# Kernel tuning notes

Hardware: AMD Instinct MI355X
Metric: run time of the kernel (lower is better)

The kernel has to match this reference:

```python
import jax, jax.numpy as jnp
import numpy as np

MAX_LAB = 64  # cap on connected-component ids per sample (original cc3d is unbounded)
BIG = jnp.int32(2 ** 30)


def _cc_label(mask):
    """26-connectivity connected components of a 3D bool mask via label propagation.
    Each component ends with label == max initial voxel id in it (nonzero), bg = 0."""
    n = mask.size
    init = jnp.where(mask, jnp.arange(1, n + 1, dtype=jnp.int32).reshape(mask.shape), jnp.int32(0))

    def cond(st):
        return jnp.any(st[0] != st[1])

    def body(st):
        lab = st[0]
        # max over 3x3x3 neighborhood == 26-connectivity propagation step
        neigh = jax.lax.reduce_window(lab, jnp.int32(0), jax.lax.max, (3, 3, 3), (1, 1, 1), 'SAME')
        return (jnp.where(mask, neigh, jnp.int32(0)), lab)

    lab, _ = jax.lax.while_loop(cond, body, (init, jnp.full_like(init, -1)))
    return lab


def _compact(lab):
    """Relabel a per-sample label map to consecutive ids 0,1..k (0 = background),
    matching cc3d's 1..k numbering."""
    u = jnp.unique(lab, size=MAX_LAB + 1, fill_value=BIG)  # sorted: [0, l1, .., lk, BIG..]
    return jnp.searchsorted(u, lab).astype(jnp.int32)


def _instance_dice(x, y):
    xb = jnp.squeeze(x, 1) > 0.5  # [B,D,H,W] pred foreground
    yb = jnp.squeeze(y, 1) > 0.5  # [B,D,H,W] gt foreground
    label = jax.vmap(lambda m: _compact(_cc_label(m)))
    gt_lab = label(yb)  # per-sample ids 0..k_i (ids shared across batch, as in original)
    pr_lab = label(xb)
    M = MAX_LAB + 1
    # joint histogram over (gt component id, pred component id), global across batch
    idx = gt_lab.reshape(-1) * M + pr_lab.reshape(-1)
    overlap = jax.ops.segment_sum(jnp.ones(idx.shape, jnp.float32), idx, num_segments=M * M).reshape(M, M)
    gt_size = overlap.sum(1)  # [M] voxels per gt id
    pr_size = overlap.sum(0)  # [M] voxels per pred id
    ov = overlap[1:, 1:]                       # [G,P] fg-fg overlaps
    inter_mask = ov > 0                        # pred comp p intersects gt comp g
    inter = ov.sum(1)                          # [G] |gt_g  ∩  union(intersecting preds)|
    union_sz = (inter_mask * pr_size[1:]).sum(1)  # [G] |union of intersecting pred comps|
    has_inter = inter > 0
    dice = jnp.where(has_inter, 2.0 * inter / jnp.maximum(union_sz + gt_size[1:], 1.0), 0.0)
    lesion_dice = dice.sum()
    num_gt = jnp.sum(gt_size[1:] > 0).astype(jnp.float32)
    tp_mask = inter_mask.any(0)                # [P] pred comps matched to some gt
    num_fp = jnp.sum((pr_size[1:] > 0) & ~tp_mask).astype(jnp.float32)
    return lesion_dice / (num_gt + num_fp)


def setup_inputs() -> dict:
    B, D, H, W = 2, 128, 128, 128
    R, N_BLOBS = 5, 12
    rng = np.random.default_rng(0)
    zz, yy, xx = np.meshgrid(np.arange(D), np.arange(H), np.arange(W), indexing='ij')

    def blobs(k):
        m = np.zeros((B, D, H, W), bool)
        for b in range(B):
            c = rng.integers(R + 2, D - R - 2, size=(k, 3))
            for cz, cy, cx in c:
                m[b] |= (zz - cz) ** 2 + (yy - cy) ** 2 + (xx - cx) ** 2 <= R * R
        return m

    y = blobs(N_BLOBS)
    # prediction = slightly shifted gt (partial-overlap TPs) + extra false-positive blobs
    x = np.roll(y, shift=(2, 1, 0), axis=(1, 2, 3)) | blobs(4)
    return {"x": jnp.asarray(x[:, None].astype(np.float32)),
            "y": jnp.asarray(y[:, None].astype(np.float32))}


def reference(x, y):
    return _instance_dice(x, y)
```

## Files before the change

### kernel.cpp

```cpp
#include <hip/hip_runtime.h>


#define NVOX (128 * 128 * 128)
#define NTOT (2 * NVOX)
#define NBLK 4096
#define CAP 12288
#define ML 65
#define NSLAB 8
#define ZSLAB 16
#define EDGE_CAP 8192
#define OVBLK 48

__global__ __launch_bounds__(256) void k_count(
    const float4* __restrict__ x, const float4* __restrict__ y,
    unsigned char* __restrict__ maskArr, int* __restrict__ blkCnt,
    int* __restrict__ overlap, int* __restrict__ cnt) {
    int t = blockIdx.x * 256 + threadIdx.x;
    float4 xv = x[t];
    float4 yv = y[t];
    unsigned m = 0;
    if (xv.x > 0.5f) m |= 1u;
    if (xv.y > 0.5f) m |= 2u;
    if (xv.z > 0.5f) m |= 4u;
    if (xv.w > 0.5f) m |= 8u;
    if (yv.x > 0.5f) m |= 16u;
    if (yv.y > 0.5f) m |= 32u;
    if (yv.z > 0.5f) m |= 64u;
    if (yv.w > 0.5f) m |= 128u;
    maskArr[t] = (unsigned char)m;
    int v = __popc(m & 0xFu) | (__popc(m >> 4) << 16);
    #pragma unroll
    for (int d = 1; d < 64; d <<= 1) v += __shfl_xor(v, d);
    __shared__ int ws[4];
    if ((threadIdx.x & 63) == 0) ws[threadIdx.x >> 6] = v;
    __syncthreads();
    if (threadIdx.x == 0) blkCnt[blockIdx.x] = ws[0] + ws[1] + ws[2] + ws[3];
    if (blockIdx.x == 0) {
        for (int i = threadIdx.x; i < ML * ML; i += 256) overlap[i] = 0;
        if (threadIdx.x < 16) cnt[8 + threadIdx.x] = 0;
    }
}

__global__ __launch_bounds__(256) void k_fill(
    const unsigned char* __restrict__ maskArr, const int* __restrict__ blkCnt,
    int* __restrict__ blkOff, int* __restrict__ cnt,
    unsigned short* __restrict__ posMapX, unsigned short* __restrict__ posMapY,
    int* __restrict__ lists) {
    int blk = blockIdx.x;
    int tid = threadIdx.x;
    int lane = tid & 63, wave = tid >> 6;

    int A = 0, B = 0, C = 0;
    #pragma unroll
    for (int k = 0; k < 4; ++k) {
        int4 c4 = ((const int4*)blkCnt)[tid * 4 + k];
        int i0 = tid * 16 + k * 4;
        const int* cc = &c4.x;
        #pragma unroll
        for (int j = 0; j < 4; ++j) {
            int c = cc[j];
            int i = i0 + j;
            C += c;
            if (i < 2048) B += c;
            if (i < blk)  A += c;
        }
    }
    #pragma unroll
    for (int d = 1; d < 64; d <<= 1) {
        A += __shfl_xor(A, d);
        B += __shfl_xor(B, d);
        C += __shfl_xor(C, d);
    }
    __shared__ int rA[4], rB[4], rC[4];
    if (lane == 0) { rA[wave] = A; rB[wave] = B; rC[wave] = C; }
    __syncthreads();
    A = rA[0] + rA[1] + rA[2] + rA[3];
    B = rB[0] + rB[1] + rB[2] + rB[3];
    C = rC[0] + rC[1] + rC[2] + rC[3];
    int base = A - (blk >= 2048 ? B : 0);
    if (tid == 0) {
        blkOff[blk] = base;
        if (blk == 0) {
            cnt[0] = B & 0xFFFF;
            cnt[2] = B >> 16;
            cnt[1] = (C & 0xFFFF) - (B & 0xFFFF);
            cnt[3] = (C >> 16)    - (B >> 16);
        }
    }

    int t = blk * 256 + tid;
    int b = blk >> 11;
    unsigned m = maskArr[t];
    int px = __popc(m & 0xFu), py = __popc(m >> 4);
    int v = px | (py << 16);
    #pragma unroll
    for (int d = 1; d < 64; d <<= 1) {
        int u = __shfl_up(v, d);
        if (lane >= d) v += u;
    }
    __shared__ int wsum[4];
    if (lane == 63) wsum[wave] = v;
    __syncthreads();
    int woff = 0;
    for (int k = 0; k < wave; ++k) woff += wsum[k];
    int incl = v + woff;
    int baseX = (base & 0xFFFF) + (incl & 0xFFFF) - px;
    int baseY = (base >> 16)    + (incl >> 16)    - py;
    int i = t << 2;
    int j = i & (NVOX - 1);
    ushort4 pxv, pyv;
    unsigned short* ppx = &pxv.x;
    unsigned short* ppy = &pyv.x;
    int cx = 0, cy = 0;
    #pragma unroll
    for (int k = 0; k < 4; ++k) {
        unsigned short vx = 0, vy = 0;
        if (m & (1u << k)) {
            int pos = baseX + cx++;
            if (pos < CAP) { lists[(0 + b) * CAP + pos] = j + k; vx = (unsigned short)(pos + 1); }
        }
        if (m & (1u << (k + 4))) {
            int pos = baseY + cy++;
            if (pos < CAP) { lists[(2 + b) * CAP + pos] = j + k; vy = (unsigned short)(pos + 1); }
        }
        ppx[k] = vx;
        ppy[k] = vy;
    }
    ((ushort4*)posMapX)[t] = pxv;
    ((ushort4*)posMapY)[t] = pyv;
}

__device__ __forceinline__ int find_root(volatile unsigned* parent, int i) {
    unsigned p = parent[i];
    while (p != (unsigned)i) {
        unsigned gp = parent[p];
        if (gp != p) parent[i] = gp;
        i = (int)p;
        p = gp;
    }
    return i;
}

__device__ __forceinline__ void lds_union(unsigned* parentNV, int a, int b) {
    volatile unsigned* parent = (volatile unsigned*)parentNV;
    int ra = find_root(parent, a);
    int rb = find_root(parent, b);
    while (ra != rb) {
        int lo = ra < rb ? ra : rb;
        int hi = ra < rb ? rb : ra;
        unsigned old = atomicCAS(&parentNV[lo], (unsigned)lo, (unsigned)hi);
        if (old == (unsigned)lo) return;
        ra = find_root(parent, (int)old);
        rb = find_root(parent, hi);
    }
}

__device__ __forceinline__ int rank_of(const int* sortedL, int nr, int v) {
    int lo = 0, hi = nr;
    while (lo < hi) { int mid = (lo + hi) >> 1; if (sortedL[mid] < v) lo = mid + 1; else hi = mid; }
    return lo;
}

__global__ __launch_bounds__(1024) void k_cc(
    const unsigned short* __restrict__ posMapX, const unsigned short* __restrict__ posMapY,
    const int* __restrict__ lists, const int* __restrict__ blkOff,
    int* __restrict__ cnt, int* __restrict__ rootPos, int* __restrict__ edges,
    unsigned char* __restrict__ lab8) {
    int fb = blockIdx.y;
    int slab = blockIdx.x;
    int f = fb >> 1, b = fb & 1;
    const unsigned short* posMap = (f ? posMapY : posMapX) + (b << 21);
    const int* fgl = lists + fb * CAP;
    int n = cnt[fb]; if (n > CAP) n = CAP;
    int blkbase = b * 2048 + slab * 256;
    int o0 = blkOff[blkbase];
    int s0 = f ? (o0 >> 16) : (o0 & 0xFFFF);
    int s1;
    if (slab == NSLAB - 1) s1 = n;
    else { int o1 = blkOff[blkbase + 256]; s1 = f ? (o1 >> 16) : (o1 & 0xFFFF); }
    if (s1 > n) s1 = n;
    int ns = s1 - s0;

    __shared__ unsigned parent[CAP];
    __shared__ int slabRoots[1024];
    __shared__ int rootsL[128];
    __shared__ int sortedL[64];
    __shared__ int nsrSh, nrSh, lastFlag;
    int tid = threadIdx.x;
    int lane = tid & 63;

    if (ns > 0) {
        int iters = (ns + 1023) >> 10;

        for (int it = 0; it < iters; ++it) {
            int q = it * 1024 + tid;
            if (q < ns) {
                int p = s0 + q;
                int j = fgl[p];
                unsigned par = (unsigned)q;
                if (p + 1 < s1 && (j & 127) != 127) {
                    if (fgl[p + 1] == j + 1) par = (unsigned)(q + 1);
                }
                parent[q] = par;
            }
        }
        __syncthreads();

        for (int it = 0; it < iters; ++it) {
            int q = it * 1024 + tid;
            bool active = q < ns;
            int j = active ? fgl[s0 + q] : -2;
            int z = j >> 14, y = (j >> 7) & 127, x0 = j & 127;
            bool ztop = active && ((z & (ZSLAB - 1)) == (ZSLAB - 1));
            unsigned short qv[12];
            int idx = 0;
            #pragma unroll
            for (int dx = -1; dx <= 1; ++dx) {
                int yy = y + 1, xx = x0 + dx;
                bool ok = active && yy <= 127 && (unsigned)xx <= 127u;
                int nj = (z << 14) + (yy << 7) + xx;
                qv[idx++] = ok ? posMap[nj] : (unsigned short)0;
            }
            #pragma unroll
            for (int dy = -1; dy <= 1; ++dy)
                #pragma unroll
                for (int dx = -1; dx <= 1; ++dx) {
                    int zz = z + 1, yy = y + dy, xx = x0 + dx;
                    bool ok = active && zz <= 127 && (unsigned)yy <= 127u && (unsigned)xx <= 127u;
                    int nj = (zz << 14) + (yy << 7) + xx;
                    qv[idx++] = ok ? posMap[nj] : (unsigned short)0;
                }
            int jprev = __shfl_up(j, 1);
            bool head = (lane == 0) || !active || ((j & 127) == 0) || (jprev != j - 1);

            int ec = 0;
            int myE[6];
            if (active) {
                {
                    int a = qv[0], bq = qv[1], c = qv[2];
                    if (head) {
                        if (a) lds_union(parent, q, a - 1 - s0);
                        else if (bq) lds_union(parent, q, bq - 1 - s0);
                    }
                    if (c && !bq) lds_union(parent, q, c - 1 - s0);
                }
                if (!ztop) {
                    #pragma unroll
                    for (int r = 1; r < 4; ++r) {
                        int a = qv[r * 3], bq = qv[r * 3 + 1], c = qv[r * 3 + 2];
                        if (head) {
                            if (a) lds_union(parent, q, a - 1 - s0);
                            else if (bq) lds_union(parent, q, bq - 1 - s0);
                        }
                        if (c && !bq) lds_union(parent, q, c - 1 - s0);
                    }
                } else {
                    #pragma unroll
                    for (int r = 1; r < 4; ++r) {
                        int a = qv[r * 3], bq = qv[r * 3 + 1], c = qv[r * 3 + 2];
                        if (head) {
                            if (a) myE[ec++] = (s0 + q) | ((a - 1) << 14);
                            else if (bq) myE[ec++] = (s0 + q) | ((bq - 1) << 14);
                        }
                        if (c && !bq) myE[ec++] = (s0 + q) | ((c - 1) << 14);
                    }
                }
            }
            int pref = ec;
            #pragma unroll
            for (int d = 1; d < 64; d <<= 1) {
                int u = __shfl_up(pref, d);
                if (lane >= d) pref += u;
            }
            int total = __shfl(pref, 63);
            if (total > 0) {
                int ebase = 0;
                if (lane == 63) ebase = atomicAdd(cnt + 8 + fb, total);
                ebase = __shfl(ebase, 63);
                int o = ebase + pref - ec;
                for (int k = 0; k < ec; ++k)
                    if (o + k < EDGE_CAP) edges[fb * EDGE_CAP + o + k] = myE[k];
            }
        }
        __syncthreads();

        for (int it = 0; it < iters; ++it) {
            int q = it * 1024 + tid;
            if (q < ns)
                rootPos[fb * CAP + s0 + q] = s0 + find_root((volatile unsigned*)parent, q);
        }
    }
    __syncthreads();

    if (tid == 0) {
        __threadfence();
        lastFlag = (atomicAdd(&cnt[16 + fb], 1) == NSLAB - 1) ? 1 : 0;
        nsrSh = 0; nrSh = 0;
    }
    __syncthreads();
    if (!lastFlag) return;
    __threadfence();

    int ne = atomicAdd(cnt + 8 + fb, 0);
    if (ne > EDGE_CAP) ne = EDGE_CAP;

    for (int p = tid; p < n; p += 1024) {
        unsigned r = (unsigned)rootPos[fb * CAP + p];
        parent[p] = r;
        if (r == (unsigned)p) {
            int s = atomicAdd(&nsrSh, 1);
            if (s < 1024) slabRoots[s] = p;
        }
    }
    __syncthreads();

    for (int e = tid; e < ne; e += 1024) {
        int pk = edges[fb * EDGE_CAP + e];
        lds_union(parent, pk & 0x3FFF, pk >> 14);
    }
    __syncthreads();

    int nsr = nsrSh; if (nsr > 1024) nsr = 1024;
    for (int i = tid; i < nsr; i += 1024) {
        int r = slabRoots[i];
        if (parent[r] == (unsigned)r) {
            int s = atomicAdd(&nrSh, 1);
            if (s < 128) rootsL[s] = r;
        }
    }
    __syncthreads();
    int nr = nrSh; if (nr > 64) nr = 64;
    if (tid < nr) {
        int v = rootsL[tid];
        int r = 0;
        for (int k = 0; k < nr; ++k) r += (rootsL[k] < v) ? 1 : 0;
        sortedL[r] = v;
    }
    __syncthreads();

    for (int i = tid; i < nsr; i += 1024) {
        int r = slabRoots[i];
        int fr = find_root((volatile unsigned*)parent, r);
        lab8[fb * CAP + r] = (unsigned char)(1 + rank_of(sortedL, nr, fr));
    }
}

__device__ __forceinline__ void hist_add_pred(int* ovl, int key, bool valid) {
    unsigned long long remaining = __ballot(valid ? 1 : 0);
    int lane = threadIdx.x & 63;
    while (remaining) {
        int leader = __ffsll(remaining) - 1;
        int lkey = __shfl(key, leader);
        unsigned long long m = __ballot((valid && lkey == key) ? 1 : 0) & remaining;
        if (lane == leader) atomicAdd(&ovl[lkey], (int)__popcll(m));
        remaining &= ~m;
    }
}

__global__ __launch_bounds__(256) void k_overlap_final(
    const unsigned short* __restrict__ posMapX, const unsigned short* __restrict__ posMapY,
    const int* __restrict__ lists, int* __restrict__ cnt,
    const int* __restrict__ rootPos, const unsigned char* __restrict__ lab8,
    int* __restrict__ overlap, float* __restrict__ out) {
    int fb = blockIdx.y;
    int f = fb >> 1, b = fb & 1;
    int n = cnt[fb]; if (n > CAP) n = CAP;
    int t = blockIdx.x * 256 + threadIdx.x;
    bool valid = t < n;
    int key = 0;
    if (valid) {
        int j = lists[fb * CAP + t];
        int gi = (b << 21) + j;
        if (f == 0) {
            int pc = (int)lab8[fb * CAP + rootPos[fb * CAP + t]];
            int q = (int)posMapY[gi];
            int gc = 0;
            if (q) gc = (int)lab8[(2 + b) * CAP + rootPos[(2 + b) * CAP + (q - 1)]];
            key = gc * ML + pc;
        } else {
            if (posMapX[gi] != 0) valid = false;
            else {
                int gc = (int)lab8[fb * CAP + rootPos[fb * CAP + t]];
                key = gc * ML;
            }
        }
    }
    hist_add_pred(overlap, key, valid);

    __shared__ int lastFlag;
    __syncthreads();
    if (threadIdx.x == 0) {
        __threadfence();
        lastFlag = (atomicAdd(&cnt[12], 1) == 4 * OVBLK - 1) ? 1 : 0;
    }
    __syncthreads();
    if (!lastFlag) return;

    __shared__ int O[ML * ML];
    __shared__ float prs[ML];
    __shared__ unsigned char tp[ML];
    __shared__ float diceSh[ML];
    __shared__ int ngSh[ML];
    __shared__ int nfSh[ML];
    int tid = threadIdx.x;
    for (int i = tid; i < ML * ML; i += 256) O[i] = overlap[i];
    __syncthreads();
    if (tid < ML) {
        int s = 0; int any = 0;
        for (int g = 0; g < ML; ++g) {
            int o = O[g * ML + tid];
            s += o;
            if (g >= 1 && o > 0) any = 1;
        }
        prs[tid] = (float)s;
        tp[tid] = (unsigned char)any;
    }
    __syncthreads();
    if (tid < ML) {
        float dice = 0.f; int ng = 0, nf = 0;
        if (tid >= 1) {
            int gt = 0, inter = 0; float un = 0.f;
            for (int p = 0; p < ML; ++p) {
                int o = O[tid * ML + p];
                gt += o;
                if (p >= 1) { inter += o; if (o > 0) un += prs[p]; }
            }
            if (inter > 0) {
                float den = un + (float)gt;
                if (den < 1.f) den = 1.f;
                dice = 2.f * (float)inter / den;
            }
            ng = (gt > 0) ? 1 : 0;
            nf = (prs[tid] > 0.f && tp[tid] == 0) ? 1 : 0;
        }
        diceSh[tid] = dice; ngSh[tid] = ng; nfSh[tid] = nf;
    }
    __syncthreads();
    if (tid == 0) {
        float ld = 0.f; int ng = 0, nf = 0;
        for (int k = 1; k < ML; ++k) { ld += diceSh[k]; ng += ngSh[k]; nf += nfSh[k]; }
        out[0] = ld / (float)(ng + nf);
    }
}

extern "C" void kernel_launch(void* const* d_in, const int* in_sizes, int n_in,
                              void* d_out, int out_size, void* d_ws, size_t ws_size,
                              hipStream_t stream) {
    const float* x = (const float*)d_in[0];
    const float* y = (const float*)d_in[1];
    float* out = (float*)d_out;

    char* base = (char*)d_ws;
    int* cnt            = (int*)base;
    int* overlap        = cnt + 32;
    int* blkCnt         = overlap + ML * ML;
    int* blkOff         = blkCnt + NBLK;
    int* lists          = blkOff + NBLK;
    int* rootPos        = lists + 4 * CAP;
    int* edges          = rootPos + 4 * CAP;
    unsigned char* lab8 = (unsigned char*)(edges + 4 * EDGE_CAP);
    unsigned char* maskArr = lab8 + 4 * CAP;
    size_t off = (size_t)((maskArr + NTOT / 4) - (unsigned char*)base);
    off = (off + 15) & ~(size_t)15;
    unsigned short* posMapX = (unsigned short*)(base + off);
    unsigned short* posMapY = posMapX + NTOT;

    k_count<<<NBLK, 256, 0, stream>>>((const float4*)x, (const float4*)y,
                                      maskArr, blkCnt, overlap, cnt);
    k_fill<<<NBLK, 256, 0, stream>>>(maskArr, blkCnt, blkOff, cnt,
                                     posMapX, posMapY, lists);
    k_cc<<<dim3(NSLAB, 4), 1024, 0, stream>>>(posMapX, posMapY, lists, blkOff,
                                              cnt, rootPos, edges, lab8);
    k_overlap_final<<<dim3(OVBLK, 4), 256, 0, stream>>>(
        posMapX, posMapY, lists, cnt, rootPos, lab8, overlap, out);
}
```

Baseline: 150.2 us.

## Split CC into finer-slab local kernel and separate merge kernel

```diff
diff --git a/kernel.cpp b/kernel.cpp
--- a/kernel.cpp
+++ b/kernel.cpp
@@ -6,8 +6,9 @@
 #define NBLK 4096
 #define CAP 12288
 #define ML 65
-#define NSLAB 8
-#define ZSLAB 16
+#define NSLAB 16
+#define ZSLAB 8
+#define SLABBLK 128
 #define EDGE_CAP 8192
 #define OVBLK 48
 
@@ -161,149 +162,146 @@
     return lo;
 }
 
-__global__ __launch_bounds__(1024) void k_cc(
+__global__ __launch_bounds__(512) void k_cc_local(
     const unsigned short* __restrict__ posMapX, const unsigned short* __restrict__ posMapY,
     const int* __restrict__ lists, const int* __restrict__ blkOff,
-    int* __restrict__ cnt, int* __restrict__ rootPos, int* __restrict__ edges,
-    unsigned char* __restrict__ lab8) {
+    int* __restrict__ cnt, int* __restrict__ rootPos, int* __restrict__ edges) {
     int fb = blockIdx.y;
     int slab = blockIdx.x;
     int f = fb >> 1, b = fb & 1;
     const unsigned short* posMap = (f ? posMapY : posMapX) + (b << 21);
     const int* fgl = lists + fb * CAP;
     int n = cnt[fb]; if (n > CAP) n = CAP;
-    int blkbase = b * 2048 + slab * 256;
+    int blkbase = b * 2048 + slab * SLABBLK;
     int o0 = blkOff[blkbase];
     int s0 = f ? (o0 >> 16) : (o0 & 0xFFFF);
     int s1;
     if (slab == NSLAB - 1) s1 = n;
-    else { int o1 = blkOff[blkbase + 256]; s1 = f ? (o1 >> 16) : (o1 & 0xFFFF); }
+    else { int o1 = blkOff[blkbase + SLABBLK]; s1 = f ? (o1 >> 16) : (o1 & 0xFFFF); }
     if (s1 > n) s1 = n;
     int ns = s1 - s0;
+    if (ns <= 0) return;
 
     __shared__ unsigned parent[CAP];
-    __shared__ int slabRoots[1024];
-    __shared__ int rootsL[128];
-    __shared__ int sortedL[64];
-    __shared__ int nsrSh, nrSh, lastFlag;
     int tid = threadIdx.x;
     int lane = tid & 63;
-
-    if (ns > 0) {
-        int iters = (ns + 1023) >> 10;
-
-        for (int it = 0; it < iters; ++it) {
-            int q = it * 1024 + tid;
-            if (q < ns) {
-                int p = s0 + q;
-                int j = fgl[p];
-                unsigned par = (unsigned)q;
-                if (p + 1 < s1 && (j & 127) != 127) {
-                    if (fgl[p + 1] == j + 1) par = (unsigned)(q + 1);
-                }
-                parent[q] = par;
-            }
-        }
-        __syncthreads();
-
-        for (int it = 0; it < iters; ++it) {
-            int q = it * 1024 + tid;
-            bool active = q < ns;
-            int j = active ? fgl[s0 + q] : -2;
-            int z = j >> 14, y = (j >> 7) & 127, x0 = j & 127;
-            bool ztop = active && ((z & (ZSLAB - 1)) == (ZSLAB - 1));
-            unsigned short qv[12];
-            int idx = 0;
+    int iters = (ns + 511) >> 9;
+
+    for (int it = 0; it < iters; ++it) {
+        int q = it * 512 + tid;
+        if (q < ns) {
+            int p = s0 + q;
+            int j = fgl[p];
+            unsigned par = (unsigned)q;
+            if (p + 1 < s1 && (j & 127) != 127) {
+                if (fgl[p + 1] == j + 1) par = (unsigned)(q + 1);
+            }
+            parent[q] = par;
+        }
+    }
+    __syncthreads();
+
+    for (int it = 0; it < iters; ++it) {
+        int q = it * 512 + tid;
+        bool active = q < ns;
+        int j = active ? fgl[s0 + q] : -2;
+        int z = j >> 14, y = (j >> 7) & 127, x0 = j & 127;
+        bool ztop = active && ((z & (ZSLAB - 1)) == (ZSLAB - 1));
+        unsigned short qv[12];
+        int idx = 0;
+        #pragma unroll
+        for (int dx = -1; dx <= 1; ++dx) {
+            int yy = y + 1, xx = x0 + dx;
+            bool ok = active && yy <= 127 && (unsigned)xx <= 127u;
+            int nj = (z << 14) + (yy << 7) + xx;
+            qv[idx++] = ok ? posMap[nj] : (unsigned short)0;
+        }
+        #pragma unroll
+        for (int dy = -1; dy <= 1; ++dy)
             #pragma unroll
             for (int dx = -1; dx <= 1; ++dx) {
-                int yy = y + 1, xx = x0 + dx;
-                bool ok = active && yy <= 127 && (unsigned)xx <= 127u;
-                int nj = (z << 14) + (yy << 7) + xx;
+                int zz = z + 1, yy = y + dy, xx = x0 + dx;
+                bool ok = active && zz <= 127 && (unsigned)yy <= 127u && (unsigned)xx <= 127u;
+                int nj = (zz << 14) + (yy << 7) + xx;
                 qv[idx++] = ok ? posMap[nj] : (unsigned short)0;
             }
-            #pragma unroll
-            for (int dy = -1; dy <= 1; ++dy)
+        int jprev = __shfl_up(j, 1);
+        bool head = (lane == 0) || !active || ((j & 127) == 0) || (jprev != j - 1);
+
+        int ec = 0;
+        int myE[6];
+        if (active) {
+            {
+                int a = qv[0], bq = qv[1], c = qv[2];
+                if (head) {
+                    if (a) lds_union(parent, q, a - 1 - s0);
+                    else if (bq) lds_union(parent, q, bq - 1 - s0);
+                }
+                if (c && !bq) lds_union(parent, q, c - 1 - s0);
+            }
+            if (!ztop) {
                 #pragma unroll
-                for (int dx = -1; dx <= 1; ++dx) {
-                    int zz = z + 1, yy = y + dy, xx = x0 + dx;
-                    bool ok = active && zz <= 127 && (unsigned)yy <= 127u && (unsigned)xx <= 127u;
-                    int nj = (zz << 14) + (yy << 7) + xx;
-                    qv[idx++] = ok ? posMap[nj] : (unsigned short)0;
-                }
-            int jprev = __shfl_up(j, 1);
-            bool head = (lane == 0) || !active || ((j & 127) == 0) || (jprev != j - 1);
-
-            int ec = 0;
-            int myE[6];
-            if (active) {
-                {
-                    int a = qv[0], bq = qv[1], c = qv[2];
+                for (int r = 1; r < 4; ++r) {
+                    int a = qv[r * 3], bq = qv[r * 3 + 1], c = qv[r * 3 + 2];
                     if (head) {
                         if (a) lds_union(parent, q, a - 1 - s0);
                         else if (bq) lds_union(parent, q, bq - 1 - s0);
                     }
                     if (c && !bq) lds_union(parent, q, c - 1 - s0);
                 }
-                if (!ztop) {
-                    #pragma unroll
-                    for (int r = 1; r < 4; ++r) {
-                        int a = qv[r * 3], bq = qv[r * 3 + 1], c = qv[r * 3 + 2];
-                        if (head) {
-                            if (a) lds_union(parent, q, a - 1 - s0);
-                            else if (bq) lds_union(parent, q, bq - 1 - s0);
-                        }
-                        if (c && !bq) lds_union(parent, q, c - 1 - s0);
+            } else {
+                #pragma unroll
+                for (int r = 1; r < 4; ++r) {
+                    int a = qv[r * 3], bq = qv[r * 3 + 1], c = qv[r * 3 + 2];
+                    if (head) {
+                        if (a) myE[ec++] = (s0 + q) | ((a - 1) << 14);
+                        else if (bq) myE[ec++] = (s0 + q) | ((bq - 1) << 14);
                     }
-                } else {
-                    #pragma unroll
-                    for (int r = 1; r < 4; ++r) {
-                        int a = qv[r * 3], bq = qv[r * 3 + 1], c = qv[r * 3 + 2];
-                        if (head) {
-                            if (a) myE[ec++] = (s0 + q) | ((a - 1) << 14);
-                            else if (bq) myE[ec++] = (s0 + q) | ((bq - 1) << 14);
-                        }
-                        if (c && !bq) myE[ec++] = (s0 + q) | ((c - 1) << 14);
-                    }
+                    if (c && !bq) myE[ec++] = (s0 + q) | ((c - 1) << 14);
                 }
             }
-            int pref = ec;
-            #pragma unroll
-            for (int d = 1; d < 64; d <<= 1) {
-                int u = __shfl_up(pref, d);
-                if (lane >= d) pref += u;
-            }
-            int total = __shfl(pref, 63);
-            if (total > 0) {
-                int ebase = 0;
-                if (lane == 63) ebase = atomicAdd(cnt + 8 + fb, total);
-                ebase = __shfl(ebase, 63);
-                int o = ebase + pref - ec;
-                for (int k = 0; k < ec; ++k)
-                    if (o + k < EDGE_CAP) edges[fb * EDGE_CAP + o + k] = myE[k];
-            }
-        }
-        __syncthreads();
-
-        for (int it = 0; it < iters; ++it) {
-            int q = it * 1024 + tid;
-            if (q < ns)
-                rootPos[fb * CAP + s0 + q] = s0 + find_root((volatile unsigned*)parent, q);
-        }
-    }
-    __syncthreads();
-
-    if (tid == 0) {
-        __threadfence();
-        lastFlag = (atomicAdd(&cnt[16 + fb], 1) == NSLAB - 1) ? 1 : 0;
-        nsrSh = 0; nrSh = 0;
-    }
-    __syncthreads();
-    if (!lastFlag) return;
-    __threadfence();
-
-    int ne = atomicAdd(cnt + 8 + fb, 0);
-    if (ne > EDGE_CAP) ne = EDGE_CAP;
-
+        }
+        int pref = ec;
+        #pragma unroll
+        for (int d = 1; d < 64; d <<= 1) {
+            int u = __shfl_up(pref, d);
+            if (lane >= d) pref += u;
+        }
+        int total = __shfl(pref, 63);
+        if (total > 0) {
+            int ebase = 0;
+            if (lane == 63) ebase = atomicAdd(cnt + 8 + fb, total);
+            ebase = __shfl(ebase, 63);
+            int o = ebase + pref - ec;
+            for (int k = 0; k < ec; ++k)
+                if (o + k < EDGE_CAP) edges[fb * EDGE_CAP + o + k] = myE[k];
+        }
+    }
+    __syncthreads();
+
+    for (int it = 0; it < iters; ++it) {
+        int q = it * 512 + tid;
+        if (q < ns)
+            rootPos[fb * CAP + s0 + q] = s0 + find_root((volatile unsigned*)parent, q);
+    }
+}
+
+__global__ __launch_bounds__(1024) void k_cc_merge(
+    const int* __restrict__ cnt, const int* __restrict__ rootPos,
+    const int* __restrict__ edges, unsigned char* __restrict__ lab8) {
+    int fb = blockIdx.x;
+    int tid = threadIdx.x;
+    int n = cnt[fb]; if (n > CAP) n = CAP;
+    int ne = cnt[8 + fb]; if (ne > EDGE_CAP) ne = EDGE_CAP;
+
+    __shared__ unsigned parent[CAP];
+    __shared__ int slabRoots[1024];
+    __shared__ int rootsL[128];
+    __shared__ int sortedL[64];
+    __shared__ int nsrSh, nrSh;
+
+    if (tid == 0) { nsrSh = 0; nrSh = 0; }
+    __syncthreads();
     for (int p = tid; p < n; p += 1024) {
         unsigned r = (unsigned)rootPos[fb * CAP + p];
         parent[p] = r;
@@ -469,8 +467,9 @@
                                       maskArr, blkCnt, overlap, cnt);
     k_fill<<<NBLK, 256, 0, stream>>>(maskArr, blkCnt, blkOff, cnt,
                                      posMapX, posMapY, lists);
-    k_cc<<<dim3(NSLAB, 4), 1024, 0, stream>>>(posMapX, posMapY, lists, blkOff,
-                                              cnt, rootPos, edges, lab8);
+    k_cc_local<<<dim3(NSLAB, 4), 512, 0, stream>>>(posMapX, posMapY, lists,
+                                                   blkOff, cnt, rootPos, edges);
+    k_cc_merge<<<4, 1024, 0, stream>>>(cnt, rootPos, edges, lab8);
     k_overlap_final<<<dim3(OVBLK, 4), 256, 0, stream>>>(
         posMapX, posMapY, lists, cnt, rootPos, lab8, overlap, out);
 }
```

After: 152.9 us. About the same (+1.8%).
